# Optimization experiments

Measured on AMD Instinct MI355X. Metric: run time of the kernel, lower is better.

The kernel has to match this reference:

```python
import jax, jax.numpy as jnp
import numpy as np

H = 100  # hidden size


def _lstm_final_hidden(x, W_ih, W_hh, b_ih, b_hh):
    # x: [B, T, 4] -> final hidden state h_T: [B, H]
    B, T, _ = x.shape
    # Precompute input contribution for all time steps: [B, T, 4H]
    xW = jnp.einsum('btf,gf->btg', x, W_ih) + b_ih + b_hh
    xW = jnp.transpose(xW, (1, 0, 2))  # [T, B, 4H] for scan over time

    def step(carry, xt):
        h, c = carry
        gates = xt + h @ W_hh.T  # [B, 4H]
        i, f, g, o = jnp.split(gates, 4, axis=-1)  # torch gate order: i, f, g, o
        c = jax.nn.sigmoid(f) * c + jax.nn.sigmoid(i) * jnp.tanh(g)
        h = jax.nn.sigmoid(o) * jnp.tanh(c)
        return (h, c), None

    h0 = jnp.zeros((B, H), dtype=x.dtype)
    (hT, _), _ = jax.lax.scan(step, (h0, h0), xW)
    return hT


def setup_inputs() -> dict:
    key = jax.random.key(0)
    k1, k2, k3, k4, k5 = jax.random.split(key, 5)
    n_cells, T = 4096, 128
    short_ttf = jax.random.normal(k1, (n_cells, 3, T, 4), dtype=jnp.float32)
    W_ih = jax.random.normal(k2, (4 * H, 4), dtype=jnp.float32) * 0.1
    # torch init: uniform(-0.05, 0.05) for weight_hh
    W_hh = jax.random.uniform(k3, (4 * H, H), dtype=jnp.float32, minval=-0.05, maxval=0.05)
    b_ih = jax.random.normal(k4, (4 * H,), dtype=jnp.float32) * 0.1
    b_hh = jax.random.normal(k5, (4 * H,), dtype=jnp.float32) * 0.1
    return {"short_ttf": short_ttf, "W_ih": W_ih, "W_hh": W_hh, "b_ih": b_ih, "b_hh": b_hh}


def reference(short_ttf, W_ih, W_hh, b_ih, b_hh):
    # short_ttf: [n_cells, 3, T, 4]. Each of the 3 sub-sequences per cell is run
    # through the same LSTM; last-step hidden states are concatenated -> [n_cells, 3H].
    n_cells, three, T, F = short_ttf.shape
    x = short_ttf.reshape(n_cells * three, T, F)  # batch all sequences together
    hT = _lstm_final_hidden(x, W_ih, W_hh, b_ih, b_hh)  # [n_cells*3, H]
    return hT.reshape(n_cells, three * H)  # [n_cells, 300]
```

## Files before the change

### kernel.cpp

```cpp
#include <hip/hip_runtime.h>
#include <cstdint>


#define H_UNITS 100
#define T_STEPS 128
#define S_BLK   16
#define NSEQ    12288
#define NBLK    (NSEQ / S_BLK)
#define NTILE   25
#define KSTR    136
#define LOG2E   1.4426950408889634f

typedef __attribute__((ext_vector_type(8))) _Float16 halfx8;
typedef __attribute__((ext_vector_type(8))) unsigned short ushortx8;
typedef __attribute__((ext_vector_type(4))) float floatx4;

__device__ __forceinline__ unsigned short f32_to_f16u(float x) {
    _Float16 h = (_Float16)x;
    return __builtin_bit_cast(unsigned short, h);
}
__device__ __forceinline__ float f16u_to_f32(unsigned short u) {
    _Float16 h = __builtin_bit_cast(_Float16, u);
    return (float)h;
}
#if __has_builtin(__builtin_amdgcn_exp2f)
__device__ __forceinline__ float fexp2(float x) { return __builtin_amdgcn_exp2f(x); }
#else
__device__ __forceinline__ float fexp2(float x) { return exp2f(x); }
#endif

__global__ void lstm_prep_pack(const float* __restrict__ W_ih,
                               const float* __restrict__ W_hh,
                               const float* __restrict__ b_ih,
                               const float* __restrict__ b_hh,
                               ushortx8* __restrict__ Bpack) {
    int t = blockIdx.x * 256 + threadIdx.x;
    if (t >= NTILE * 4 * 64) return;
    int lane = t & 63;
    int kc   = (t >> 6) & 3;
    int tile = t >> 8;
    int m    = lane & 15;
    int n  = (m & 3) * 100 + tile * 4 + (m >> 2);
    float sc = (n >= 200 && n < 300) ? (2.0f * LOG2E) : LOG2E;
    int k0 = kc * 32 + ((lane >> 4) & 3) * 8;
    ushortx8 v;
#pragma unroll
    for (int j = 0; j < 8; ++j) {
        int k = k0 + j;
        unsigned short w = 0;
        if (k < 100) {
            w = f32_to_f16u(W_hh[n * 100 + k] * sc);
        } else if (k < 108) {
            w = f32_to_f16u(W_ih[n * 4 + ((k - 100) & 3)] * sc);
        } else if (k < 112) {
            float wf = W_ih[n * 4 + (k - 108)] * sc;
            unsigned short hi = f32_to_f16u(wf);
            w = f32_to_f16u(wf - f16u_to_f32(hi));
        } else if (k == 112) {
            float b = (b_ih[n] + b_hh[n]) * sc;
            w = f32_to_f16u(b);
        } else if (k == 113) {
            float b = (b_ih[n] + b_hh[n]) * sc;
            unsigned short hi = f32_to_f16u(b);
            w = f32_to_f16u(b - f16u_to_f32(hi));
        }
        v[j] = w;
    }
    Bpack[t] = v;
}

__global__ void __launch_bounds__(256, 3)
lstm_main(const float* __restrict__ x, const ushortx8* __restrict__ Bpack,
          float* __restrict__ out) {
    __shared__ __align__(16) unsigned short s_A[2][16 * KSTR];
    __shared__ __align__(16) ushortx8       s_W[NTILE * 64];

    const int tid  = threadIdx.x;
    const int lane = tid & 63;
    const int wave = tid >> 6;
    const int seq0 = blockIdx.x * S_BLK;
    const int m    = lane & 15;
    const int quad = lane >> 4;

    halfx8 wfrag[7][3];
#pragma unroll
    for (int it = 0; it < 7; ++it) {
        int tile = wave + it * 4;
        if (tile < NTILE) {
#pragma unroll
            for (int kc = 0; kc < 3; ++kc)
                wfrag[it][kc] = __builtin_bit_cast(halfx8, Bpack[(tile * 4 + kc + 1) * 64 + lane]);
        }
    }
    for (int i = tid; i < NTILE * 64; i += 256)
        s_W[i] = Bpack[(i >> 6) * 256 + (i & 63)];

    const int rt = tid - 128;
    const int rs = rt & 15, rc = (rt >> 4) & 7;
    const float* xb = x + (size_t)(seq0 + rs) * (T_STEPS * 4) + (rc & 3);

    for (int i = tid; i < (2 * 16 * KSTR) / 2; i += 256)
        ((unsigned int*)s_A)[i] = 0u;
    float x0 = 0.0f;
    if (tid >= 128) x0 = xb[0];
    __syncthreads();
    if (tid >= 128) {
        if (rc < 4) {
            unsigned short hi = f32_to_f16u(x0);
            s_A[0][rs * KSTR + 100 + rc] = hi;
            s_A[0][rs * KSTR + 108 + rc] = hi;
        } else {
            unsigned short hi = f32_to_f16u(x0);
            s_A[0][rs * KSTR + 104 + (rc - 4)] = f32_to_f16u(x0 - f16u_to_f32(hi));
        }
    } else if (tid < 32) {
        s_A[tid >> 4][(tid & 15) * KSTR + 112] = 0x3C00;
    } else if (tid < 64) {
        int d = tid - 32;
        s_A[d >> 4][(d & 15) * KSTR + 113] = 0x3C00;
    }

    float c_reg[6];
#pragma unroll
    for (int it = 0; it < 6; ++it) c_reg[it] = 0.0f;
    float c24 = 0.0f;

    const int aOff = m * KSTR + quad * 8;

    for (int t = 0; t < T_STEPS; ++t) {
        const int bR = t & 1;
        float xnext = 0.0f;
        if (tid >= 128) {
            int tn = t + 1; if (tn > T_STEPS - 1) tn = T_STEPS - 1;
            xnext = xb[tn * 4];
        }
        __syncthreads();

        const unsigned short* base  = s_A[bR];
        unsigned short*       baseW = s_A[bR ^ 1];
        halfx8 hh[4];
#pragma unroll
        for (int kc = 0; kc < 4; ++kc)
            hh[kc] = *(const halfx8*)(base + aOff + kc * 32);

        const bool last = (t == T_STEPS - 1);

        auto docell = [&](int tile, halfx8 w1, halfx8 w2, halfx8 w3, float& cm) {
            halfx8 w0 = __builtin_bit_cast(halfx8, s_W[tile * 64 + lane]);
            floatx4 acc = {0.0f, 0.0f, 0.0f, 0.0f};
            acc = __builtin_amdgcn_mfma_f32_16x16x32_f16(w0, hh[0], acc, 0, 0, 0);
            acc = __builtin_amdgcn_mfma_f32_16x16x32_f16(w1, hh[1], acc, 0, 0, 0);
            acc = __builtin_amdgcn_mfma_f32_16x16x32_f16(w2, hh[2], acc, 0, 0, 0);
            acc = __builtin_amdgcn_mfma_f32_16x16x32_f16(w3, hh[3], acc, 0, 0, 0);
            float ei = fexp2(acc[0]);
            float ef = fexp2(acc[1]);
            float eg = fexp2(acc[2]);
            float eo = fexp2(acc[3]);
            float a  = 1.0f + ei, b = 1.0f + ef;
            float d  = eg + 1.0f, e2 = eg - 1.0f;
            float q  = a * d;
            float r  = __builtin_amdgcn_rcpf(q * b);
            float nm = fmaf(ef * q, cm, (ei * b * (2.0f * LOG2E)) * e2);
            float c2 = nm * r;
            cm = c2;
            float cc = fminf(c2, 115.0f);
            float ec = fexp2(cc);
            float r2 = __builtin_amdgcn_rcpf((1.0f + eo) * (ec + 1.0f));
            float h  = (eo * (ec - 1.0f)) * r2;
            int j = tile * 4 + quad;
            if (!last) {
                baseW[m * KSTR + j] = f32_to_f16u(h);
            } else {
                out[(size_t)(seq0 + m) * H_UNITS + j] = h;
            }
        };

#pragma unroll
        for (int it = 0; it < 6; ++it)
            docell(wave + it * 4, wfrag[it][0], wfrag[it][1], wfrag[it][2], c_reg[it]);
        if (wave == 0)
            docell(24, wfrag[6][0], wfrag[6][1], wfrag[6][2], c24);

        if (tid >= 128 && !last) {
            if (rc < 4) {
                unsigned short hi = f32_to_f16u(xnext);
                baseW[rs * KSTR + 100 + rc] = hi;
                baseW[rs * KSTR + 108 + rc] = hi;
            } else {
                unsigned short hi = f32_to_f16u(xnext);
                baseW[rs * KSTR + 104 + (rc - 4)] = f32_to_f16u(xnext - f16u_to_f32(hi));
            }
        }
        __syncthreads();
    }
}

extern "C" void kernel_launch(void* const* d_in, const int* in_sizes, int n_in,
                              void* d_out, int out_size, void* d_ws, size_t ws_size,
                              hipStream_t stream) {
    const float* x    = (const float*)d_in[0];
    const float* W_ih = (const float*)d_in[1];
    const float* W_hh = (const float*)d_in[2];
    const float* b_ih = (const float*)d_in[3];
    const float* b_hh = (const float*)d_in[4];
    ushortx8* Bpack = (ushortx8*)d_ws;

    lstm_prep_pack<<<25, 256, 0, stream>>>(W_ih, W_hh, b_ih, b_hh, Bpack);
    lstm_main<<<NBLK, 256, 0, stream>>>(x, Bpack, (float*)d_out);
}
```

Baseline: 294.8 us.

## Permute hidden-state K layout and drop one barrier per timestep

Permutes the K ordering of the packed weights and the shared-memory A rows, so that the h values two tiles write land in interleaved slots of each 8-element chunk, with x and bias terms moved to new offsets. This is meant to spread the 16-bit LDS writes and avoid bank conflicts. The barrier at the top of each timestep is replaced by a single barrier after init, leaving one sync per step. It also makes the wave index uniform via readfirstlane and folds the 2*log2e scale into an FMA. The layout change must stay consistent between the pack kernel and the main kernel, which adds correctness risk.

```diff
diff --git a/kernel.cpp b/kernel.cpp
--- a/kernel.cpp
+++ b/kernel.cpp
@@ -10,6 +10,7 @@
 #define NTILE   25
 #define KSTR    136
 #define LOG2E   1.4426950408889634f
+#define TWO_L   2.8853900817779268f
 
 typedef __attribute__((ext_vector_type(8))) _Float16 halfx8;
 typedef __attribute__((ext_vector_type(8))) unsigned short ushortx8;
@@ -48,21 +49,31 @@
     for (int j = 0; j < 8; ++j) {
         int k = k0 + j;
         unsigned short w = 0;
-        if (k < 100) {
-            w = f32_to_f16u(W_hh[n * 100 + k] * sc);
-        } else if (k < 108) {
-            w = f32_to_f16u(W_ih[n * 4 + ((k - 100) & 3)] * sc);
+        if (k < 96) {
+            int u = ((k >> 3) << 3) + ((k & 1) << 2) + ((k & 7) >> 1);
+            w = f32_to_f16u(W_hh[n * 100 + u] * sc);
+        } else if (k < 104) {
+            if (!(k & 1)) {
+                int u = 96 + ((k - 96) >> 1);
+                w = f32_to_f16u(W_hh[n * 100 + u] * sc);
+            }
         } else if (k < 112) {
-            float wf = W_ih[n * 4 + (k - 108)] * sc;
-            unsigned short hi = f32_to_f16u(wf);
-            w = f32_to_f16u(wf - f16u_to_f32(hi));
-        } else if (k == 112) {
-            float b = (b_ih[n] + b_hh[n]) * sc;
-            w = f32_to_f16u(b);
-        } else if (k == 113) {
-            float b = (b_ih[n] + b_hh[n]) * sc;
-            unsigned short hi = f32_to_f16u(b);
-            w = f32_to_f16u(b - f16u_to_f32(hi));
+            int c = (k - 104) >> 1;
+            w = f32_to_f16u(W_ih[n * 4 + c] * sc);
+        } else if (k < 120) {
+            if (!(k & 1)) {
+                int c = (k - 112) >> 1;
+                float wf = W_ih[n * 4 + c] * sc;
+                unsigned short hi = f32_to_f16u(wf);
+                w = f32_to_f16u(wf - f16u_to_f32(hi));
+            }
+        } else if (k == 120) {
+            float bb = (b_ih[n] + b_hh[n]) * sc;
+            w = f32_to_f16u(bb);
+        } else if (k == 122) {
+            float bb = (b_ih[n] + b_hh[n]) * sc;
+            unsigned short hi = f32_to_f16u(bb);
+            w = f32_to_f16u(bb - f16u_to_f32(hi));
         }
         v[j] = w;
     }
@@ -77,7 +88,7 @@
 
     const int tid  = threadIdx.x;
     const int lane = tid & 63;
-    const int wave = tid >> 6;
+    const int wavu = __builtin_amdgcn_readfirstlane(tid >> 6);
     const int seq0 = blockIdx.x * S_BLK;
     const int m    = lane & 15;
     const int quad = lane >> 4;
@@ -85,7 +96,7 @@
     halfx8 wfrag[7][3];
 #pragma unroll
     for (int it = 0; it < 7; ++it) {
-        int tile = wave + it * 4;
+        int tile = wavu + it * 4;
         if (tile < NTILE) {
 #pragma unroll
             for (int kc = 0; kc < 3; ++kc)
@@ -105,39 +116,48 @@
     if (tid >= 128) x0 = xb[0];
     __syncthreads();
     if (tid >= 128) {
+        unsigned short hi = f32_to_f16u(x0);
         if (rc < 4) {
-            unsigned short hi = f32_to_f16u(x0);
-            s_A[0][rs * KSTR + 100 + rc] = hi;
-            s_A[0][rs * KSTR + 108 + rc] = hi;
+            s_A[0][rs * KSTR + 104 + 2 * rc] = hi;
+            s_A[0][rs * KSTR + 112 + 2 * rc] = hi;
         } else {
-            unsigned short hi = f32_to_f16u(x0);
-            s_A[0][rs * KSTR + 104 + (rc - 4)] = f32_to_f16u(x0 - f16u_to_f32(hi));
+            s_A[0][rs * KSTR + 105 + 2 * (rc - 4)] =
+                f32_to_f16u(x0 - f16u_to_f32(hi));
         }
     } else if (tid < 32) {
-        s_A[tid >> 4][(tid & 15) * KSTR + 112] = 0x3C00;
+        s_A[tid >> 4][(tid & 15) * KSTR + 120] = 0x3C00;
     } else if (tid < 64) {
         int d = tid - 32;
-        s_A[d >> 4][(d & 15) * KSTR + 113] = 0x3C00;
-    }
+        s_A[d >> 4][(d & 15) * KSTR + 122] = 0x3C00;
+    }
+    __syncthreads();
 
     float c_reg[6];
 #pragma unroll
     for (int it = 0; it < 6; ++it) c_reg[it] = 0.0f;
     float c24 = 0.0f;
 
-    const int aOff = m * KSTR + quad * 8;
+    const int rowOff = m * KSTR;
+    const int aOff   = rowOff + quad * 8;
+    const int q2     = quad << 1;
+    int hbase[7];
+#pragma unroll
+    for (int it = 0; it < 7; ++it) {
+        int tile = wavu + it * 4;
+        hbase[it] = (tile < 24) ? (((tile >> 1) << 3) + (tile & 1)) : 96;
+    }
 
     for (int t = 0; t < T_STEPS; ++t) {
         const int bR = t & 1;
+        const unsigned short* base  = s_A[bR];
+        unsigned short*       baseW = s_A[bR ^ 1];
+
         float xnext = 0.0f;
         if (tid >= 128) {
             int tn = t + 1; if (tn > T_STEPS - 1) tn = T_STEPS - 1;
             xnext = xb[tn * 4];
         }
-        __syncthreads();
-
-        const unsigned short* base  = s_A[bR];
-        unsigned short*       baseW = s_A[bR ^ 1];
+
         halfx8 hh[4];
 #pragma unroll
         for (int kc = 0; kc < 4; ++kc)
@@ -145,7 +165,7 @@
 
         const bool last = (t == T_STEPS - 1);
 
-        auto docell = [&](int tile, halfx8 w1, halfx8 w2, halfx8 w3, float& cm) {
+        auto docell = [&](int tile, int wbase, halfx8 w1, halfx8 w2, halfx8 w3, float& cm) {
             halfx8 w0 = __builtin_bit_cast(halfx8, s_W[tile * 64 + lane]);
             floatx4 acc = {0.0f, 0.0f, 0.0f, 0.0f};
             acc = __builtin_amdgcn_mfma_f32_16x16x32_f16(w0, hh[0], acc, 0, 0, 0);
@@ -157,38 +177,39 @@
             float eg = fexp2(acc[2]);
             float eo = fexp2(acc[3]);
             float a  = 1.0f + ei, b = 1.0f + ef;
-            float d  = eg + 1.0f, e2 = eg - 1.0f;
+            float d  = eg + 1.0f;
+            float e2s = fmaf(eg, TWO_L, -TWO_L);
             float q  = a * d;
             float r  = __builtin_amdgcn_rcpf(q * b);
-            float nm = fmaf(ef * q, cm, (ei * b * (2.0f * LOG2E)) * e2);
+            float nm = fmaf(ef * q, cm, (ei * b) * e2s);
             float c2 = nm * r;
             cm = c2;
             float cc = fminf(c2, 115.0f);
             float ec = fexp2(cc);
             float r2 = __builtin_amdgcn_rcpf((1.0f + eo) * (ec + 1.0f));
             float h  = (eo * (ec - 1.0f)) * r2;
-            int j = tile * 4 + quad;
             if (!last) {
-                baseW[m * KSTR + j] = f32_to_f16u(h);
+                baseW[rowOff + wbase + q2] = f32_to_f16u(h);
             } else {
+                int j = tile * 4 + quad;
                 out[(size_t)(seq0 + m) * H_UNITS + j] = h;
             }
         };
 
 #pragma unroll
         for (int it = 0; it < 6; ++it)
-            docell(wave + it * 4, wfrag[it][0], wfrag[it][1], wfrag[it][2], c_reg[it]);
-        if (wave == 0)
-            docell(24, wfrag[6][0], wfrag[6][1], wfrag[6][2], c24);
+            docell(wavu + it * 4, hbase[it], wfrag[it][0], wfrag[it][1], wfrag[it][2], c_reg[it]);
+        if (wavu == 0)
+            docell(24, hbase[6], wfrag[6][0], wfrag[6][1], wfrag[6][2], c24);
 
         if (tid >= 128 && !last) {
+            unsigned short hi = f32_to_f16u(xnext);
             if (rc < 4) {
-                unsigned short hi = f32_to_f16u(xnext);
-                baseW[rs * KSTR + 100 + rc] = hi;
-                baseW[rs * KSTR + 108 + rc] = hi;
+                baseW[rs * KSTR + 104 + 2 * rc] = hi;
+                baseW[rs * KSTR + 112 + 2 * rc] = hi;
             } else {
-                unsigned short hi = f32_to_f16u(xnext);
-                baseW[rs * KSTR + 104 + (rc - 4)] = f32_to_f16u(xnext - f16u_to_f32(hi));
+                baseW[rs * KSTR + 105 + 2 * (rc - 4)] =
+                    f32_to_f16u(xnext - f16u_to_f32(hi));
             }
         }
         __syncthreads();
```

After: 286.7 us. 2.7% less time.

## Pair gate tiles to vectorize LSTM activations with packed float2 math

Applied to the files above, without the earlier changes.

Reorders the packed weight rows so each pair of MFMA tiles yields the i,f,g,o gates for two hidden units per lane. The activation math can then run on float2 vectors, which may map to packed FP32 instructions, and each lane writes its two f16 h values as a single 32-bit store. The wave index is made uniform with readfirstlane, and one of the two barriers per timestep is dropped by hoisting a single barrier before the loop. The goal is fewer VALU instructions and LDS stores on the serial recurrence path, at the cost of a more intricate weight layout.

```diff
diff --git a/kernel.cpp b/kernel.cpp
--- a/kernel.cpp
+++ b/kernel.cpp
@@ -10,10 +10,12 @@
 #define NTILE   25
 #define KSTR    136
 #define LOG2E   1.4426950408889634f
+#define TWO_L   2.8853900817779268f
 
 typedef __attribute__((ext_vector_type(8))) _Float16 halfx8;
 typedef __attribute__((ext_vector_type(8))) unsigned short ushortx8;
 typedef __attribute__((ext_vector_type(4))) float floatx4;
+typedef __attribute__((ext_vector_type(2))) float floatx2;
 
 __device__ __forceinline__ unsigned short f32_to_f16u(float x) {
     _Float16 h = (_Float16)x;
@@ -40,7 +42,16 @@
     int kc   = (t >> 6) & 3;
     int tile = t >> 8;
     int m    = lane & 15;
-    int n  = (m & 3) * 100 + tile * 4 + (m >> 2);
+    int n;
+    if (tile < 24) {
+        int pr = tile >> 1, half = tile & 1;
+        int reg = m & 3,   qr   = m >> 2;
+        int g = (reg >> 1) + 2 * half;
+        int u = 8 * pr + 2 * qr + (reg & 1);
+        n = g * 100 + u;
+    } else {
+        n = (m & 3) * 100 + 96 + (m >> 2);
+    }
     float sc = (n >= 200 && n < 300) ? (2.0f * LOG2E) : LOG2E;
     int k0 = kc * 32 + ((lane >> 4) & 3) * 8;
     ushortx8 v;
@@ -57,12 +68,12 @@
             unsigned short hi = f32_to_f16u(wf);
             w = f32_to_f16u(wf - f16u_to_f32(hi));
         } else if (k == 112) {
-            float b = (b_ih[n] + b_hh[n]) * sc;
-            w = f32_to_f16u(b);
+            float bb = (b_ih[n] + b_hh[n]) * sc;
+            w = f32_to_f16u(bb);
         } else if (k == 113) {
-            float b = (b_ih[n] + b_hh[n]) * sc;
-            unsigned short hi = f32_to_f16u(b);
-            w = f32_to_f16u(b - f16u_to_f32(hi));
+            float bb = (b_ih[n] + b_hh[n]) * sc;
+            unsigned short hi = f32_to_f16u(bb);
+            w = f32_to_f16u(bb - f16u_to_f32(hi));
         }
         v[j] = w;
     }
@@ -77,20 +88,24 @@
 
     const int tid  = threadIdx.x;
     const int lane = tid & 63;
-    const int wave = tid >> 6;
+    const int wavu = __builtin_amdgcn_readfirstlane(tid >> 6);
     const int seq0 = blockIdx.x * S_BLK;
     const int m    = lane & 15;
     const int quad = lane >> 4;
+    const int q2   = quad << 1;
 
     halfx8 wfrag[7][3];
 #pragma unroll
-    for (int it = 0; it < 7; ++it) {
-        int tile = wave + it * 4;
-        if (tile < NTILE) {
-#pragma unroll
-            for (int kc = 0; kc < 3; ++kc)
-                wfrag[it][kc] = __builtin_bit_cast(halfx8, Bpack[(tile * 4 + kc + 1) * 64 + lane]);
-        }
+    for (int s = 0; s < 6; ++s) {
+        int tile = 2 * (wavu + (s >> 1) * 4) + (s & 1);
+#pragma unroll
+        for (int kc = 0; kc < 3; ++kc)
+            wfrag[s][kc] = __builtin_bit_cast(halfx8, Bpack[(tile * 4 + kc + 1) * 64 + lane]);
+    }
+    if (wavu == 0) {
+#pragma unroll
+        for (int kc = 0; kc < 3; ++kc)
+            wfrag[6][kc] = __builtin_bit_cast(halfx8, Bpack[(24 * 4 + kc + 1) * 64 + lane]);
     }
     for (int i = tid; i < NTILE * 64; i += 256)
         s_W[i] = Bpack[(i >> 6) * 256 + (i & 63)];
@@ -105,13 +120,13 @@
     if (tid >= 128) x0 = xb[0];
     __syncthreads();
     if (tid >= 128) {
+        unsigned short hi = f32_to_f16u(x0);
         if (rc < 4) {
-            unsigned short hi = f32_to_f16u(x0);
             s_A[0][rs * KSTR + 100 + rc] = hi;
             s_A[0][rs * KSTR + 108 + rc] = hi;
         } else {
-            unsigned short hi = f32_to_f16u(x0);
-            s_A[0][rs * KSTR + 104 + (rc - 4)] = f32_to_f16u(x0 - f16u_to_f32(hi));
+            s_A[0][rs * KSTR + 104 + (rc - 4)] =
+                f32_to_f16u(x0 - f16u_to_f32(hi));
         }
     } else if (tid < 32) {
         s_A[tid >> 4][(tid & 15) * KSTR + 112] = 0x3C00;
@@ -119,25 +134,27 @@
         int d = tid - 32;
         s_A[d >> 4][(d & 15) * KSTR + 113] = 0x3C00;
     }
-
-    float c_reg[6];
-#pragma unroll
-    for (int it = 0; it < 6; ++it) c_reg[it] = 0.0f;
+    __syncthreads();
+
+    floatx2 cpr[3];
+#pragma unroll
+    for (int it = 0; it < 3; ++it) cpr[it] = (floatx2){0.0f, 0.0f};
     float c24 = 0.0f;
 
-    const int aOff = m * KSTR + quad * 8;
+    const int rowOff = m * KSTR;
+    const int aOff   = rowOff + quad * 8;
 
     for (int t = 0; t < T_STEPS; ++t) {
         const int bR = t & 1;
+        const unsigned short* base  = s_A[bR];
+        unsigned short*       baseW = s_A[bR ^ 1];
+
         float xnext = 0.0f;
         if (tid >= 128) {
             int tn = t + 1; if (tn > T_STEPS - 1) tn = T_STEPS - 1;
             xnext = xb[tn * 4];
         }
-        __syncthreads();
-
-        const unsigned short* base  = s_A[bR];
-        unsigned short*       baseW = s_A[bR ^ 1];
+
         halfx8 hh[4];
 #pragma unroll
         for (int kc = 0; kc < 4; ++kc)
@@ -145,50 +162,95 @@
 
         const bool last = (t == T_STEPS - 1);
 
-        auto docell = [&](int tile, halfx8 w1, halfx8 w2, halfx8 w3, float& cm) {
-            halfx8 w0 = __builtin_bit_cast(halfx8, s_W[tile * 64 + lane]);
-            floatx4 acc = {0.0f, 0.0f, 0.0f, 0.0f};
-            acc = __builtin_amdgcn_mfma_f32_16x16x32_f16(w0, hh[0], acc, 0, 0, 0);
-            acc = __builtin_amdgcn_mfma_f32_16x16x32_f16(w1, hh[1], acc, 0, 0, 0);
-            acc = __builtin_amdgcn_mfma_f32_16x16x32_f16(w2, hh[2], acc, 0, 0, 0);
-            acc = __builtin_amdgcn_mfma_f32_16x16x32_f16(w3, hh[3], acc, 0, 0, 0);
+        auto gemm4 = [&](halfx8 w0, const halfx8* w123) {
+            floatx4 a = {0.0f, 0.0f, 0.0f, 0.0f};
+            a = __builtin_amdgcn_mfma_f32_16x16x32_f16(w0,      hh[0], a, 0, 0, 0);
+            a = __builtin_amdgcn_mfma_f32_16x16x32_f16(w123[0], hh[1], a, 0, 0, 0);
+            a = __builtin_amdgcn_mfma_f32_16x16x32_f16(w123[1], hh[2], a, 0, 0, 0);
+            a = __builtin_amdgcn_mfma_f32_16x16x32_f16(w123[2], hh[3], a, 0, 0, 0);
+            return a;
+        };
+
+        auto activatePair = [&](floatx4 aA, floatx4 aB, floatx2& cm, int p) {
+            floatx2 ei = {fexp2(aA[0]), fexp2(aA[1])};
+            floatx2 ef = {fexp2(aA[2]), fexp2(aA[3])};
+            floatx2 eg = {fexp2(aB[0]), fexp2(aB[1])};
+            floatx2 eo = {fexp2(aB[2]), fexp2(aB[3])};
+            floatx2 a  = ei + 1.0f;
+            floatx2 b  = ef + 1.0f;
+            floatx2 d  = eg + 1.0f;
+            floatx2 p1 = eo + 1.0f;
+            floatx2 e2s = eg * TWO_L - TWO_L;
+            floatx2 q  = a * d;
+            floatx2 qb = q * b;
+            floatx2 r  = {__builtin_amdgcn_rcpf(qb[0]), __builtin_amdgcn_rcpf(qb[1])};
+            floatx2 eib = ei * b;
+            floatx2 efq = ef * q;
+            floatx2 tt  = eib * e2s;
+            floatx2 nm  = efq * cm + tt;
+            floatx2 c2  = nm * r;
+            cm = c2;
+            floatx2 cc = {fminf(c2[0], 115.0f), fminf(c2[1], 115.0f)};
+            floatx2 ec = {fexp2(cc[0]), fexp2(cc[1])};
+            floatx2 p2 = ec + 1.0f;
+            floatx2 nu = ec - 1.0f;
+            floatx2 pp = p1 * p2;
+            floatx2 r2 = {__builtin_amdgcn_rcpf(pp[0]), __builtin_amdgcn_rcpf(pp[1])};
+            floatx2 eon = eo * nu;
+            floatx2 hv  = eon * r2;
+            if (!last) {
+                unsigned int pk = (unsigned int)f32_to_f16u(hv[0]) |
+                                  ((unsigned int)f32_to_f16u(hv[1]) << 16);
+                *(unsigned int*)&baseW[rowOff + 8 * p + q2] = pk;
+            } else {
+                *(floatx2*)&out[(size_t)(seq0 + m) * H_UNITS + 8 * p + q2] = hv;
+            }
+        };
+
+#pragma unroll
+        for (int it = 0; it < 3; ++it) {
+            int p = wavu + it * 4;
+            halfx8 w0A = __builtin_bit_cast(halfx8, s_W[(2 * p) * 64 + lane]);
+            halfx8 w0B = __builtin_bit_cast(halfx8, s_W[(2 * p + 1) * 64 + lane]);
+            floatx4 aA = gemm4(w0A, wfrag[2 * it]);
+            floatx4 aB = gemm4(w0B, wfrag[2 * it + 1]);
+            activatePair(aA, aB, cpr[it], p);
+        }
+
+        if (wavu == 0) {
+            halfx8 w0 = __builtin_bit_cast(halfx8, s_W[24 * 64 + lane]);
+            floatx4 acc = gemm4(w0, wfrag[6]);
             float ei = fexp2(acc[0]);
             float ef = fexp2(acc[1]);
             float eg = fexp2(acc[2]);
             float eo = fexp2(acc[3]);
             float a  = 1.0f + ei, b = 1.0f + ef;
-            float d  = eg + 1.0f, e2 = eg - 1.0f;
+            float d  = eg + 1.0f;
+            float e2s = fmaf(eg, TWO_L, -TWO_L);
             float q  = a * d;
             float r  = __builtin_amdgcn_rcpf(q * b);
-            float nm = fmaf(ef * q, cm, (ei * b * (2.0f * LOG2E)) * e2);
+            float nm = fmaf(ef * q, c24, (ei * b) * e2s);
             float c2 = nm * r;
-            cm = c2;
+            c24 = c2;
             float cc = fminf(c2, 115.0f);
             float ec = fexp2(cc);
             float r2 = __builtin_amdgcn_rcpf((1.0f + eo) * (ec + 1.0f));
             float h  = (eo * (ec - 1.0f)) * r2;
-            int j = tile * 4 + quad;
             if (!last) {
-                baseW[m * KSTR + j] = f32_to_f16u(h);
+                baseW[rowOff + 96 + quad] = f32_to_f16u(h);
             } else {
-                out[(size_t)(seq0 + m) * H_UNITS + j] = h;
+                out[(size_t)(seq0 + m) * H_UNITS + 96 + quad] = h;
             }
-        };
-
-#pragma unroll
-        for (int it = 0; it < 6; ++it)
-            docell(wave + it * 4, wfrag[it][0], wfrag[it][1], wfrag[it][2], c_reg[it]);
-        if (wave == 0)
-            docell(24, wfrag[6][0], wfrag[6][1], wfrag[6][2], c24);
+        }
 
         if (tid >= 128 && !last) {
+            unsigned short hi = f32_to_f16u(xnext);
             if (rc < 4) {
-                unsigned short hi = f32_to_f16u(xnext);
                 baseW[rs * KSTR + 100 + rc] = hi;
                 baseW[rs * KSTR + 108 + rc] = hi;
             } else {
-                unsigned short hi = f32_to_f16u(xnext);
-                baseW[rs * KSTR + 104 + (rc - 4)] = f32_to_f16u(xnext - f16u_to_f32(hi));
+                baseW[rs * KSTR + 104 + (rc - 4)] =
+                    f32_to_f16u(xnext - f16u_to_f32(hi));
             }
         }
         __syncthreads();
```

New measurement: 283.5 us. 1.04x faster.
